# Optimization experiments

Measured on AMD Instinct MI355X. Metric: run time of the kernel, lower is better.

Reference implementation:

```python
import jax, jax.numpy as jnp
import numpy as np

P = 8.0  # Lp exponent of the distance neuron (finite-p stage of l_inf-dist training)


def _patches(t, k, stride, pad):
    # [B, Cin, H, W] -> [B, Cin*k*k, H', W'], feature dim ordered channel-major
    return jax.lax.conv_general_dilated_patches(
        t, (k, k), (stride, stride), [(pad, pad), (pad, pad)])


def _lp(d):
    # d: [B, Cout, Cin*k*k, H', W'] nonnegative -> Lp norm over patch dim
    return jnp.power(jnp.sum(jnp.power(d, P), axis=2), 1.0 / P)


def norm_dist_conv(x, l, u, w, stride, pad):
    # Lp-distance "convolution": y[b,o,i,j] = || patch(x)[b,:,i,j] - w[o,:] ||_p
    # mean_normalize=True: zero-center each output unit's weight vector
    Cout, Cin, k, _ = w.shape
    wf = w.reshape(Cout, -1)
    wf = wf - jnp.mean(wf, axis=1, keepdims=True)
    wb = wf[None, :, :, None, None]                      # [1, Cout, Ckk, 1, 1]
    px = _patches(x, k, stride, pad)[:, None]            # [B, 1, Ckk, H', W']
    pl = _patches(l, k, stride, pad)[:, None]
    pu = _patches(u, k, stride, pad)[:, None]
    y = _lp(jnp.abs(px - wb))
    # interval bounds of |x_j - w_j| given x_j in [l_j, u_j], then monotone Lp
    dl = jnp.maximum(jnp.maximum(pl - wb, wb - pu), 0.0)
    du = jnp.maximum(jnp.abs(pl - wb), jnp.abs(pu - wb))
    return y, _lp(dl), _lp(du)


def bound_relu(x, l, u):
    # ReLU is monotone: apply elementwise to value and both bounds
    return jax.nn.relu(x), jax.nn.relu(l), jax.nn.relu(u)


def setup_inputs() -> dict:
    key = jax.random.key(0)
    k1, k2, k3 = jax.random.split(key, 3)
    B, C, H, W = 4, 32, 32, 32
    eps = 0.1  # l_inf perturbation radius
    x = jax.random.normal(k1, (B, C, H, W), dtype=jnp.float32)
    lower = x - eps
    upper = x + eps
    scale = 1.0 / np.sqrt(C * 9)
    weight1 = jax.random.normal(k2, (C, C, 3, 3), dtype=jnp.float32) * scale
    weight2 = jax.random.normal(k3, (C, C, 3, 3), dtype=jnp.float32) * scale
    return {"x": x, "lower": lower, "upper": upper,
            "weight1": weight1, "weight2": weight2}


def reference(x, lower, upper, weight1, weight2):
    # conv1 (stride=1, pad=1) -> BoundReLU -> conv2 -> residual add -> BoundReLU
    o = norm_dist_conv(x, lower, upper, weight1, 1, 1)
    o = bound_relu(*o)
    o = norm_dist_conv(*o, weight2, 1, 1)
    out = (o[0] + x, o[1] + lower, o[2] + upper)  # identity shortcut (stride=1, in==out)
    out = bound_relu(*out)
    return jnp.stack(out)  # [3, B, C, H, W]: (value, lower, upper)
```

## Files before the change

### kernel.cpp

```cpp
#include <hip/hip_runtime.h>

#define NB 4
#define NC 32
#define NH 32
#define NW 32
#define KK 288
#define PLANE (NB*NC*NH*NW)
#define CHALF 16

__device__ __forceinline__ float s3(float v) { return sqrtf(sqrtf(sqrtf(v))); }

__global__ __launch_bounds__(256) void prep_weights_k(
        const float* __restrict__ w1, const float* __restrict__ w2,
        float* __restrict__ wf1, float* __restrict__ wf2)
{
    const int row = blockIdx.x;
    const float* src = (row < NC) ? w1 : w2;
    float* dst = (row < NC) ? wf1 : wf2;
    const int co = row & (NC - 1);
    const int tid = threadIdx.x;
    __shared__ float red[256];
    const float a = src[co*KK + tid];
    const float b = (tid + 256 < KK) ? src[co*KK + tid + 256] : 0.0f;
    red[tid] = a + b;
    __syncthreads();
    for (int s = 128; s > 0; s >>= 1) {
        if (tid < s) red[tid] += red[tid + s];
        __syncthreads();
    }
    const float mean = red[0] * (1.0f / (float)KK);
    {
        const int e = tid, c = e / 9, r9 = e - c*9, r = r9 / 3, kw = r9 - r*3;
        dst[co*384 + ((c*3 + r) << 2) + kw] = a - mean;
    }
    if (tid + 256 < KK) {
        const int e = tid + 256, c = e / 9, r9 = e - c*9, r = r9 / 3, kw = r9 - r*3;
        dst[co*384 + ((c*3 + r) << 2) + kw] = b - mean;
    }
}

template<bool STAGE2>
__global__ __launch_bounds__(256, 2) void normdist_conv_k(
    const float* __restrict__ sy,
    const float* __restrict__ sl,
    const float* __restrict__ su,
    const float* __restrict__ wf,
    float* __restrict__ pY, float* __restrict__ pL, float* __restrict__ pU)
{
    const int h     = blockIdx.x;
    const int cog   = blockIdx.y >> 1;
    const int chalf = blockIdx.y & 1;
    const int ch0   = chalf * CHALF;
    const int b     = blockIdx.z;
    const int tx    = threadIdx.x;
    const int ty    = threadIdx.y;
    const int tid   = ty * 32 + tx;

    __shared__ float4 sP[CHALF*3*34];

    for (int i = tid; i < CHALF*3*34; i += 256) {
        const int c   = i / 102;
        const int rem = i - c*102;
        const int r   = rem / 34;
        const int col = rem - r*34;
        const int gh  = h + r - 1;
        const int gw  = col - 1;
        float vx = 0.0f, vl = 0.0f, vu = 0.0f;
        if ((unsigned)gh < NH && (unsigned)gw < NW) {
            const int g = ((b*NC + ch0 + c)*NH + gh)*NW + gw;
            if (STAGE2) {
                vx = s3(sy[g] + sy[PLANE + g]);
                vl = s3(sl[g] + sl[PLANE + g]);
                vu = s3(su[g] + su[PLANE + g]);
            } else {
                vx = sy[g]; vl = sl[g]; vu = su[g];
            }
        }
        sP[i] = make_float4(vx, vl, vu, 0.0f);
    }
    __syncthreads();

    const int co0 = cog*16 + ty;
    const int co1 = co0 + 8;
    const float4* wbA = (const float4*)wf + (co0*NC + ch0)*3;
    const float4* wbB = (const float4*)wf + (co1*NC + ch0)*3;

    float aY0 = 0.0f, aL0 = 0.0f, aU0 = 0.0f;
    float aY1 = 0.0f, aL1 = 0.0f, aU1 = 0.0f;

    auto tap = [&](float wv, float4 p, float& accY, float& accL, float& accU) {
        const float d  = p.x - wv;
        const float d2 = d*d, d4 = d2*d2;
        accY = fmaf(d4, d4, accY);
        const float a  = p.y - wv;
        const float nb = wv - p.z;
        const float m  = fmaxf(fmaxf(a, nb), 0.0f);
        const float m2 = m*m, m4 = m2*m2;
        accL = fmaf(m4, m4, accL);
        const float a2 = a*a, q2 = nb*nb;
        const float mm2 = fmaxf(a2, q2);
        const float mm4 = mm2*mm2;
        accU = fmaf(mm4, mm4, accU);
    };

    float4 cA0 = wbA[0], cA1 = wbA[1], cA2 = wbA[2];
    float4 cB0 = wbB[0], cB1 = wbB[1], cB2 = wbB[2];

    for (int c = 0; c < CHALF; ++c) {
        const int cn = (c < CHALF-1) ? c + 1 : c;
        const float4 nA0 = wbA[cn*3+0], nA1 = wbA[cn*3+1], nA2 = wbA[cn*3+2];
        const float4 nB0 = wbB[cn*3+0], nB1 = wbB[cn*3+1], nB2 = wbB[cn*3+2];

        const int pb = c*102 + tx;
        const float4 p00 = sP[pb +  0], p01 = sP[pb +  1], p02 = sP[pb +  2];
        const float4 p10 = sP[pb + 34], p11 = sP[pb + 35], p12 = sP[pb + 36];
        const float4 p20 = sP[pb + 68], p21 = sP[pb + 69], p22 = sP[pb + 70];

        tap(cA0.x, p00, aY0, aL0, aU0); tap(cA0.y, p01, aY0, aL0, aU0); tap(cA0.z, p02, aY0, aL0, aU0);
        tap(cB0.x, p00, aY1, aL1, aU1); tap(cB0.y, p01, aY1, aL1, aU1); tap(cB0.z, p02, aY1, aL1, aU1);
        tap(cA1.x, p10, aY0, aL0, aU0); tap(cA1.y, p11, aY0, aL0, aU0); tap(cA1.z, p12, aY0, aL0, aU0);
        tap(cB1.x, p10, aY1, aL1, aU1); tap(cB1.y, p11, aY1, aL1, aU1); tap(cB1.z, p12, aY1, aL1, aU1);
        tap(cA2.x, p20, aY0, aL0, aU0); tap(cA2.y, p21, aY0, aL0, aU0); tap(cA2.z, p22, aY0, aL0, aU0);
        tap(cB2.x, p20, aY1, aL1, aU1); tap(cB2.y, p21, aY1, aL1, aU1); tap(cB2.z, p22, aY1, aL1, aU1);

        cA0 = nA0; cA1 = nA1; cA2 = nA2;
        cB0 = nB0; cB1 = nB1; cB2 = nB2;
    }

    const int o0 = ((b*NC + co0)*NH + h)*NW + tx;
    const int o1 = o0 + 8*NH*NW;
    pY[chalf*PLANE + o0] = aY0;
    pL[chalf*PLANE + o0] = aL0;
    pU[chalf*PLANE + o0] = aU0;
    pY[chalf*PLANE + o1] = aY1;
    pL[chalf*PLANE + o1] = aL1;
    pU[chalf*PLANE + o1] = aU1;
}

__global__ __launch_bounds__(256) void epilogue_k(
    const float* __restrict__ pY, const float* __restrict__ pL, const float* __restrict__ pU,
    const float* __restrict__ x,  const float* __restrict__ l,  const float* __restrict__ u,
    float* __restrict__ out)
{
    const int i = blockIdx.x*256 + threadIdx.x;
    const float4* pY4 = (const float4*)pY;
    const float4* pL4 = (const float4*)pL;
    const float4* pU4 = (const float4*)pU;
    const float4* x4  = (const float4*)x;
    const float4* l4  = (const float4*)l;
    const float4* u4  = (const float4*)u;
    float4* out4 = (float4*)out;
    const int Q = PLANE/4;

    const float4 ya = pY4[i], yb = pY4[Q + i];
    const float4 la = pL4[i], lb = pL4[Q + i];
    const float4 ua = pU4[i], ub = pU4[Q + i];
    const float4 xr = x4[i], lr = l4[i], ur = u4[i];

    float4 oy, ol, ou;
    oy.x = fmaxf(s3(ya.x + yb.x) + xr.x, 0.0f);
    oy.y = fmaxf(s3(ya.y + yb.y) + xr.y, 0.0f);
    oy.z = fmaxf(s3(ya.z + yb.z) + xr.z, 0.0f);
    oy.w = fmaxf(s3(ya.w + yb.w) + xr.w, 0.0f);
    ol.x = fmaxf(s3(la.x + lb.x) + lr.x, 0.0f);
    ol.y = fmaxf(s3(la.y + lb.y) + lr.y, 0.0f);
    ol.z = fmaxf(s3(la.z + lb.z) + lr.z, 0.0f);
    ol.w = fmaxf(s3(la.w + lb.w) + lr.w, 0.0f);
    ou.x = fmaxf(s3(ua.x + ub.x) + ur.x, 0.0f);
    ou.y = fmaxf(s3(ua.y + ub.y) + ur.y, 0.0f);
    ou.z = fmaxf(s3(ua.z + ub.z) + ur.z, 0.0f);
    ou.w = fmaxf(s3(ua.w + ub.w) + ur.w, 0.0f);

    out4[i]       = oy;
    out4[Q + i]   = ol;
    out4[2*Q + i] = ou;
}

extern "C" void kernel_launch(void* const* d_in, const int* in_sizes, int n_in,
                              void* d_out, int out_size, void* d_ws, size_t ws_size,
                              hipStream_t stream)
{
    const float* x  = (const float*)d_in[0];
    const float* l  = (const float*)d_in[1];
    const float* u  = (const float*)d_in[2];
    const float* w1 = (const float*)d_in[3];
    const float* w2 = (const float*)d_in[4];
    float* ws  = (float*)d_ws;
    float* wf1 = ws;
    float* wf2 = wf1 + 12288;
    float* p1Y = wf2 + 12288;
    float* p1L = p1Y + 2*PLANE;
    float* p1U = p1L + 2*PLANE;
    float* p2Y = p1U + 2*PLANE;
    float* p2L = p2Y + 2*PLANE;
    float* p2U = p2L + 2*PLANE;
    float* out = (float*)d_out;

    prep_weights_k<<<64, 256, 0, stream>>>(w1, w2, wf1, wf2);

    dim3 blk(32, 8);
    dim3 grd(NH, 4, NB);
    normdist_conv_k<false><<<grd, blk, 0, stream>>>(x, l, u, wf1, p1Y, p1L, p1U);
    normdist_conv_k<true ><<<grd, blk, 0, stream>>>(p1Y, p1L, p1U, wf2, p2Y, p2L, p2U);
    epilogue_k<<<PLANE/1024, 256, 0, stream>>>(p2Y, p2L, p2U, x, l, u, out);
}
```

Measured before the change: 108.0 us.

## Fuse all stages into one cooperative kernel with grid syncs

Combines weight prep, both distance-conv stages and the epilogue into a single cooperative launch of 256 blocks of 512 threads, separated by grid-wide syncs, to remove the cost of several kernel launches. Each block now covers all 32 output channels for one row and channel half, so the grid shrinks from 512 blocks of 256 threads to 256 blocks of 512. The epilogue becomes scalar rather than float4. If the cooperative launch fails, it falls back to separate kernels. With only 256 blocks the GPU may be underused, and grid syncs carry their own overhead.

```diff
diff --git a/kernel.cpp b/kernel.cpp
--- a/kernel.cpp
+++ b/kernel.cpp
@@ -1,4 +1,7 @@
 #include <hip/hip_runtime.h>
+#include <hip/hip_cooperative_groups.h>
+
+namespace cg = cooperative_groups;
 
 #define NB 4
 #define NC 32
@@ -7,58 +10,51 @@
 #define KK 288
 #define PLANE (NB*NC*NH*NW)
 #define CHALF 16
+#define NBLK 256
+#define NTHR 512
 
 __device__ __forceinline__ float s3(float v) { return sqrtf(sqrtf(sqrtf(v))); }
 
-__global__ __launch_bounds__(256) void prep_weights_k(
+
+__device__ __forceinline__ void prep_phase(int bid, int tid,
         const float* __restrict__ w1, const float* __restrict__ w2,
-        float* __restrict__ wf1, float* __restrict__ wf2)
-{
-    const int row = blockIdx.x;
-    const float* src = (row < NC) ? w1 : w2;
-    float* dst = (row < NC) ? wf1 : wf2;
-    const int co = row & (NC - 1);
-    const int tid = threadIdx.x;
-    __shared__ float red[256];
-    const float a = src[co*KK + tid];
-    const float b = (tid + 256 < KK) ? src[co*KK + tid + 256] : 0.0f;
-    red[tid] = a + b;
+        float* __restrict__ wf1, float* __restrict__ wf2, float* red)
+{
+    if (bid >= 2*NC) return;
+    const float* src = (bid < NC) ? w1 : w2;
+    float* dst = (bid < NC) ? wf1 : wf2;
+    const int co = bid & (NC - 1);
+    const float a = (tid < KK) ? src[co*KK + tid] : 0.0f;
+    red[tid] = a;
     __syncthreads();
-    for (int s = 128; s > 0; s >>= 1) {
+    for (int s = NTHR/2; s > 0; s >>= 1) {
         if (tid < s) red[tid] += red[tid + s];
         __syncthreads();
     }
     const float mean = red[0] * (1.0f / (float)KK);
-    {
-        const int e = tid, c = e / 9, r9 = e - c*9, r = r9 / 3, kw = r9 - r*3;
+    if (tid < KK) {
+        const int c = tid / 9, r9 = tid - c*9, r = r9 / 3, kw = r9 - r*3;
         dst[co*384 + ((c*3 + r) << 2) + kw] = a - mean;
     }
-    if (tid + 256 < KK) {
-        const int e = tid + 256, c = e / 9, r9 = e - c*9, r = r9 / 3, kw = r9 - r*3;
-        dst[co*384 + ((c*3 + r) << 2) + kw] = b - mean;
-    }
 }
 
 template<bool STAGE2>
-__global__ __launch_bounds__(256, 2) void normdist_conv_k(
+__device__ __forceinline__ void conv_phase(int bid, int tid,
     const float* __restrict__ sy,
     const float* __restrict__ sl,
     const float* __restrict__ su,
     const float* __restrict__ wf,
-    float* __restrict__ pY, float* __restrict__ pL, float* __restrict__ pU)
-{
-    const int h     = blockIdx.x;
-    const int cog   = blockIdx.y >> 1;
-    const int chalf = blockIdx.y & 1;
+    float* __restrict__ pY, float* __restrict__ pL, float* __restrict__ pU,
+    float4* sP)
+{
+    const int h     = bid & (NH - 1);
+    const int chalf = (bid >> 5) & 1;
+    const int b     = bid >> 6;
     const int ch0   = chalf * CHALF;
-    const int b     = blockIdx.z;
-    const int tx    = threadIdx.x;
-    const int ty    = threadIdx.y;
-    const int tid   = ty * 32 + tx;
-
-    __shared__ float4 sP[CHALF*3*34];
-
-    for (int i = tid; i < CHALF*3*34; i += 256) {
+    const int tx    = tid & 31;
+    const int ty    = tid >> 5;
+
+    for (int i = tid; i < CHALF*3*34; i += NTHR) {
         const int c   = i / 102;
         const int rem = i - c*102;
         const int r   = rem / 34;
@@ -80,8 +76,8 @@
     }
     __syncthreads();
 
-    const int co0 = cog*16 + ty;
-    const int co1 = co0 + 8;
+    const int co0 = ty;
+    const int co1 = ty + 16;
     const float4* wbA = (const float4*)wf + (co0*NC + ch0)*3;
     const float4* wbB = (const float4*)wf + (co1*NC + ch0)*3;
 
@@ -128,7 +124,7 @@
     }
 
     const int o0 = ((b*NC + co0)*NH + h)*NW + tx;
-    const int o1 = o0 + 8*NH*NW;
+    const int o1 = o0 + 16*NH*NW;
     pY[chalf*PLANE + o0] = aY0;
     pL[chalf*PLANE + o0] = aL0;
     pU[chalf*PLANE + o0] = aU0;
@@ -137,44 +133,76 @@
     pU[chalf*PLANE + o1] = aU1;
 }
 
-__global__ __launch_bounds__(256) void epilogue_k(
+__device__ __forceinline__ void epilogue_phase(int o,
     const float* __restrict__ pY, const float* __restrict__ pL, const float* __restrict__ pU,
     const float* __restrict__ x,  const float* __restrict__ l,  const float* __restrict__ u,
     float* __restrict__ out)
 {
-    const int i = blockIdx.x*256 + threadIdx.x;
-    const float4* pY4 = (const float4*)pY;
-    const float4* pL4 = (const float4*)pL;
-    const float4* pU4 = (const float4*)pU;
-    const float4* x4  = (const float4*)x;
-    const float4* l4  = (const float4*)l;
-    const float4* u4  = (const float4*)u;
-    float4* out4 = (float4*)out;
-    const int Q = PLANE/4;
-
-    const float4 ya = pY4[i], yb = pY4[Q + i];
-    const float4 la = pL4[i], lb = pL4[Q + i];
-    const float4 ua = pU4[i], ub = pU4[Q + i];
-    const float4 xr = x4[i], lr = l4[i], ur = u4[i];
-
-    float4 oy, ol, ou;
-    oy.x = fmaxf(s3(ya.x + yb.x) + xr.x, 0.0f);
-    oy.y = fmaxf(s3(ya.y + yb.y) + xr.y, 0.0f);
-    oy.z = fmaxf(s3(ya.z + yb.z) + xr.z, 0.0f);
-    oy.w = fmaxf(s3(ya.w + yb.w) + xr.w, 0.0f);
-    ol.x = fmaxf(s3(la.x + lb.x) + lr.x, 0.0f);
-    ol.y = fmaxf(s3(la.y + lb.y) + lr.y, 0.0f);
-    ol.z = fmaxf(s3(la.z + lb.z) + lr.z, 0.0f);
-    ol.w = fmaxf(s3(la.w + lb.w) + lr.w, 0.0f);
-    ou.x = fmaxf(s3(ua.x + ub.x) + ur.x, 0.0f);
-    ou.y = fmaxf(s3(ua.y + ub.y) + ur.y, 0.0f);
-    ou.z = fmaxf(s3(ua.z + ub.z) + ur.z, 0.0f);
-    ou.w = fmaxf(s3(ua.w + ub.w) + ur.w, 0.0f);
-
-    out4[i]       = oy;
-    out4[Q + i]   = ol;
-    out4[2*Q + i] = ou;
-}
+    const float y  = s3(pY[o] + pY[PLANE + o]);
+    const float dl = s3(pL[o] + pL[PLANE + o]);
+    const float du = s3(pU[o] + pU[PLANE + o]);
+    out[o]           = fmaxf(y  + x[o], 0.0f);
+    out[PLANE + o]   = fmaxf(dl + l[o], 0.0f);
+    out[2*PLANE + o] = fmaxf(du + u[o], 0.0f);
+}
+
+
+__global__ __launch_bounds__(NTHR, 1) void fused_k(
+    const float* __restrict__ x, const float* __restrict__ l, const float* __restrict__ u,
+    const float* __restrict__ w1, const float* __restrict__ w2,
+    float* __restrict__ wf1, float* __restrict__ wf2,
+    float* __restrict__ p1Y, float* __restrict__ p1L, float* __restrict__ p1U,
+    float* __restrict__ p2Y, float* __restrict__ p2L, float* __restrict__ p2U,
+    float* __restrict__ out)
+{
+    __shared__ float4 sP[CHALF*3*34];
+    __shared__ float red[NTHR];
+    cg::grid_group grid = cg::this_grid();
+    const int bid = blockIdx.x;
+    const int tid = threadIdx.x;
+
+    prep_phase(bid, tid, w1, w2, wf1, wf2, red);
+    __threadfence();
+    grid.sync();
+
+    conv_phase<false>(bid, tid, x, l, u, wf1, p1Y, p1L, p1U, sP);
+    __threadfence();
+    grid.sync();
+
+    conv_phase<true>(bid, tid, p1Y, p1L, p1U, wf2, p2Y, p2L, p2U, sP);
+    __threadfence();
+    grid.sync();
+
+    epilogue_phase(bid*NTHR + tid, p2Y, p2L, p2U, x, l, u, out);
+}
+
+
+__global__ __launch_bounds__(NTHR) void prep_only_k(
+        const float* __restrict__ w1, const float* __restrict__ w2,
+        float* __restrict__ wf1, float* __restrict__ wf2)
+{
+    __shared__ float red[NTHR];
+    prep_phase(blockIdx.x, threadIdx.x, w1, w2, wf1, wf2, red);
+}
+
+template<bool STAGE2>
+__global__ __launch_bounds__(NTHR) void conv_only_k(
+    const float* __restrict__ sy, const float* __restrict__ sl, const float* __restrict__ su,
+    const float* __restrict__ wf,
+    float* __restrict__ pY, float* __restrict__ pL, float* __restrict__ pU)
+{
+    __shared__ float4 sP[CHALF*3*34];
+    conv_phase<STAGE2>(blockIdx.x, threadIdx.x, sy, sl, su, wf, pY, pL, pU, sP);
+}
+
+__global__ __launch_bounds__(NTHR) void epilogue_only_k(
+    const float* __restrict__ pY, const float* __restrict__ pL, const float* __restrict__ pU,
+    const float* __restrict__ x,  const float* __restrict__ l,  const float* __restrict__ u,
+    float* __restrict__ out)
+{
+    epilogue_phase(blockIdx.x*NTHR + threadIdx.x, pY, pL, pU, x, l, u, out);
+}
+
 
 extern "C" void kernel_launch(void* const* d_in, const int* in_sizes, int n_in,
                               void* d_out, int out_size, void* d_ws, size_t ws_size,
@@ -196,11 +224,18 @@
     float* p2U = p2L + 2*PLANE;
     float* out = (float*)d_out;
 
-    prep_weights_k<<<64, 256, 0, stream>>>(w1, w2, wf1, wf2);
-
-    dim3 blk(32, 8);
-    dim3 grd(NH, 4, NB);
-    normdist_conv_k<false><<<grd, blk, 0, stream>>>(x, l, u, wf1, p1Y, p1L, p1U);
-    normdist_conv_k<true ><<<grd, blk, 0, stream>>>(p1Y, p1L, p1U, wf2, p2Y, p2L, p2U);
-    epilogue_k<<<PLANE/1024, 256, 0, stream>>>(p2Y, p2L, p2U, x, l, u, out);
-}
+    void* args[] = { (void*)&x, (void*)&l, (void*)&u, (void*)&w1, (void*)&w2,
+                     (void*)&wf1, (void*)&wf2,
+                     (void*)&p1Y, (void*)&p1L, (void*)&p1U,
+                     (void*)&p2Y, (void*)&p2L, (void*)&p2U, (void*)&out };
+
+    hipError_t err = hipLaunchCooperativeKernel((const void*)fused_k,
+                                                dim3(NBLK), dim3(NTHR), args, 0, stream);
+    if (err != hipSuccess) {
+        (void)hipGetLastError();
+        prep_only_k<<<2*NC, NTHR, 0, stream>>>(w1, w2, wf1, wf2);
+        conv_only_k<false><<<NBLK, NTHR, 0, stream>>>(x, l, u, wf1, p1Y, p1L, p1U);
+        conv_only_k<true ><<<NBLK, NTHR, 0, stream>>>(p1Y, p1L, p1U, wf2, p2Y, p2L, p2U);
+        epilogue_only_k<<<NBLK, NTHR, 0, stream>>>(p2Y, p2L, p2U, x, l, u, out);
+    }
+}
```

Result: slower. 335.0 us (+210.1%).

## Drop channel split-K and fuse Lp root plus residual epilogue into conv

Applied to the files above, without the earlier changes.

Each conv block now reduces over all 32 input channels instead of half. This removes the partial-sum buffers, the separate epilogue kernel, and the cross-half combine in stage 2's load. The 1/8 root, residual add and ReLU are applied directly when the second conv stores its result. In exchange the grid shrinks from 512 to 256 blocks, with twice the work per block and double the shared-memory tile. That lowers occupancy and may weaken latency hiding on a compute-bound loop.

```diff
diff --git a/kernel.cpp b/kernel.cpp
--- a/kernel.cpp
+++ b/kernel.cpp
@@ -6,7 +6,6 @@
 #define NW 32
 #define KK 288
 #define PLANE (NB*NC*NH*NW)
-#define CHALF 16
 
 __device__ __forceinline__ float s3(float v) { return sqrtf(sqrtf(sqrtf(v))); }
 
@@ -40,25 +39,22 @@
 }
 
 template<bool STAGE2>
-__global__ __launch_bounds__(256, 2) void normdist_conv_k(
-    const float* __restrict__ sy,
-    const float* __restrict__ sl,
-    const float* __restrict__ su,
+__global__ __launch_bounds__(256, 1) void conv_full_k(
+    const float* __restrict__ sy, const float* __restrict__ sl, const float* __restrict__ su,
     const float* __restrict__ wf,
-    float* __restrict__ pY, float* __restrict__ pL, float* __restrict__ pU)
+    const float* __restrict__ rx, const float* __restrict__ rl, const float* __restrict__ ru,
+    float* __restrict__ oY, float* __restrict__ oL, float* __restrict__ oU)
 {
-    const int h     = blockIdx.x;
-    const int cog   = blockIdx.y >> 1;
-    const int chalf = blockIdx.y & 1;
-    const int ch0   = chalf * CHALF;
-    const int b     = blockIdx.z;
-    const int tx    = threadIdx.x;
-    const int ty    = threadIdx.y;
-    const int tid   = ty * 32 + tx;
+    const int h   = blockIdx.x;
+    const int cog = blockIdx.y;
+    const int b   = blockIdx.z;
+    const int tx  = threadIdx.x;
+    const int ty  = threadIdx.y;
+    const int tid = ty * 32 + tx;
 
-    __shared__ float4 sP[CHALF*3*34];
+    __shared__ float4 sP[NC*3*34];
 
-    for (int i = tid; i < CHALF*3*34; i += 256) {
+    for (int i = tid; i < NC*3*34; i += 256) {
         const int c   = i / 102;
         const int rem = i - c*102;
         const int r   = rem / 34;
@@ -67,14 +63,8 @@
         const int gw  = col - 1;
         float vx = 0.0f, vl = 0.0f, vu = 0.0f;
         if ((unsigned)gh < NH && (unsigned)gw < NW) {
-            const int g = ((b*NC + ch0 + c)*NH + gh)*NW + gw;
-            if (STAGE2) {
-                vx = s3(sy[g] + sy[PLANE + g]);
-                vl = s3(sl[g] + sl[PLANE + g]);
-                vu = s3(su[g] + su[PLANE + g]);
-            } else {
-                vx = sy[g]; vl = sl[g]; vu = su[g];
-            }
+            const int g = ((b*NC + c)*NH + gh)*NW + gw;
+            vx = sy[g]; vl = sl[g]; vu = su[g];
         }
         sP[i] = make_float4(vx, vl, vu, 0.0f);
     }
@@ -82,8 +72,8 @@
 
     const int co0 = cog*16 + ty;
     const int co1 = co0 + 8;
-    const float4* wbA = (const float4*)wf + (co0*NC + ch0)*3;
-    const float4* wbB = (const float4*)wf + (co1*NC + ch0)*3;
+    const float4* wbA = (const float4*)wf + co0*NC*3;
+    const float4* wbB = (const float4*)wf + co1*NC*3;
 
     float aY0 = 0.0f, aL0 = 0.0f, aU0 = 0.0f;
     float aY1 = 0.0f, aL1 = 0.0f, aU1 = 0.0f;
@@ -106,8 +96,8 @@
     float4 cA0 = wbA[0], cA1 = wbA[1], cA2 = wbA[2];
     float4 cB0 = wbB[0], cB1 = wbB[1], cB2 = wbB[2];
 
-    for (int c = 0; c < CHALF; ++c) {
-        const int cn = (c < CHALF-1) ? c + 1 : c;
+    for (int c = 0; c < NC; ++c) {
+        const int cn = (c < NC-1) ? c + 1 : c;
         const float4 nA0 = wbA[cn*3+0], nA1 = wbA[cn*3+1], nA2 = wbA[cn*3+2];
         const float4 nB0 = wbB[cn*3+0], nB1 = wbB[cn*3+1], nB2 = wbB[cn*3+2];
 
@@ -129,51 +119,19 @@
 
     const int o0 = ((b*NC + co0)*NH + h)*NW + tx;
     const int o1 = o0 + 8*NH*NW;
-    pY[chalf*PLANE + o0] = aY0;
-    pL[chalf*PLANE + o0] = aL0;
-    pU[chalf*PLANE + o0] = aU0;
-    pY[chalf*PLANE + o1] = aY1;
-    pL[chalf*PLANE + o1] = aL1;
-    pU[chalf*PLANE + o1] = aU1;
-}
 
-__global__ __launch_bounds__(256) void epilogue_k(
-    const float* __restrict__ pY, const float* __restrict__ pL, const float* __restrict__ pU,
-    const float* __restrict__ x,  const float* __restrict__ l,  const float* __restrict__ u,
-    float* __restrict__ out)
-{
-    const int i = blockIdx.x*256 + threadIdx.x;
-    const float4* pY4 = (const float4*)pY;
-    const float4* pL4 = (const float4*)pL;
-    const float4* pU4 = (const float4*)pU;
-    const float4* x4  = (const float4*)x;
-    const float4* l4  = (const float4*)l;
-    const float4* u4  = (const float4*)u;
-    float4* out4 = (float4*)out;
-    const int Q = PLANE/4;
-
-    const float4 ya = pY4[i], yb = pY4[Q + i];
-    const float4 la = pL4[i], lb = pL4[Q + i];
-    const float4 ua = pU4[i], ub = pU4[Q + i];
-    const float4 xr = x4[i], lr = l4[i], ur = u4[i];
-
-    float4 oy, ol, ou;
-    oy.x = fmaxf(s3(ya.x + yb.x) + xr.x, 0.0f);
-    oy.y = fmaxf(s3(ya.y + yb.y) + xr.y, 0.0f);
-    oy.z = fmaxf(s3(ya.z + yb.z) + xr.z, 0.0f);
-    oy.w = fmaxf(s3(ya.w + yb.w) + xr.w, 0.0f);
-    ol.x = fmaxf(s3(la.x + lb.x) + lr.x, 0.0f);
-    ol.y = fmaxf(s3(la.y + lb.y) + lr.y, 0.0f);
-    ol.z = fmaxf(s3(la.z + lb.z) + lr.z, 0.0f);
-    ol.w = fmaxf(s3(la.w + lb.w) + lr.w, 0.0f);
-    ou.x = fmaxf(s3(ua.x + ub.x) + ur.x, 0.0f);
-    ou.y = fmaxf(s3(ua.y + ub.y) + ur.y, 0.0f);
-    ou.z = fmaxf(s3(ua.z + ub.z) + ur.z, 0.0f);
-    ou.w = fmaxf(s3(ua.w + ub.w) + ur.w, 0.0f);
-
-    out4[i]       = oy;
-    out4[Q + i]   = ol;
-    out4[2*Q + i] = ou;
+    if (STAGE2) {
+        oY[o0]         = fmaxf(s3(aY0) + rx[o0], 0.0f);
+        oY[o1]         = fmaxf(s3(aY1) + rx[o1], 0.0f);
+        oL[o0]         = fmaxf(s3(aL0) + rl[o0], 0.0f);
+        oL[o1]         = fmaxf(s3(aL1) + rl[o1], 0.0f);
+        oU[o0]         = fmaxf(s3(aU0) + ru[o0], 0.0f);
+        oU[o1]         = fmaxf(s3(aU1) + ru[o1], 0.0f);
+    } else {
+        oY[o0] = s3(aY0); oY[o1] = s3(aY1);
+        oL[o0] = s3(aL0); oL[o1] = s3(aL1);
+        oU[o0] = s3(aU0); oU[o1] = s3(aU1);
+    }
 }
 
 extern "C" void kernel_launch(void* const* d_in, const int* in_sizes, int n_in,
@@ -188,19 +146,19 @@
     float* ws  = (float*)d_ws;
     float* wf1 = ws;
     float* wf2 = wf1 + 12288;
-    float* p1Y = wf2 + 12288;
-    float* p1L = p1Y + 2*PLANE;
-    float* p1U = p1L + 2*PLANE;
-    float* p2Y = p1U + 2*PLANE;
-    float* p2L = p2Y + 2*PLANE;
-    float* p2U = p2L + 2*PLANE;
+    float* y1  = wf2 + 12288;
+    float* l1  = y1 + PLANE;
+    float* u1  = l1 + PLANE;
     float* out = (float*)d_out;
 
     prep_weights_k<<<64, 256, 0, stream>>>(w1, w2, wf1, wf2);
 
     dim3 blk(32, 8);
-    dim3 grd(NH, 4, NB);
-    normdist_conv_k<false><<<grd, blk, 0, stream>>>(x, l, u, wf1, p1Y, p1L, p1U);
-    normdist_conv_k<true ><<<grd, blk, 0, stream>>>(p1Y, p1L, p1U, wf2, p2Y, p2L, p2U);
-    epilogue_k<<<PLANE/1024, 256, 0, stream>>>(p2Y, p2L, p2U, x, l, u, out);
+    dim3 grd(NH, 2, NB);
+    conv_full_k<false><<<grd, blk, 0, stream>>>(x, l, u, wf1,
+                                                nullptr, nullptr, nullptr,
+                                                y1, l1, u1);
+    conv_full_k<true ><<<grd, blk, 0, stream>>>(y1, l1, u1, wf2,
+                                                x, l, u,
+                                                out, out + PLANE, out + 2*PLANE);
 }
```

New measurement: 112.1 us. 3.7% more time.

## Pack two output channels into v2f lanes for packed FP32 math

Applied to the files above, without the earlier changes.

The weight prep kernel now interleaves the weights of the paired output channels co and co+8 into adjacent slots. The inner distance loop can then run on two-wide float vectors with packed fma, mul and max, computing both channels' taps in one instruction stream. The aim is to roughly halve VALU instruction count in the compute-bound tap loop by using packed FP32 instructions. Risks are extra broadcast or move instructions, and packed max or sub lowering to scalar ops if the compiler does not emit v_pk forms for them.

```diff
diff --git a/kernel.cpp b/kernel.cpp
--- a/kernel.cpp
+++ b/kernel.cpp
@@ -8,7 +8,11 @@
 #define PLANE (NB*NC*NH*NW)
 #define CHALF 16
 
+typedef float v2f __attribute__((ext_vector_type(2)));
+
 __device__ __forceinline__ float s3(float v) { return sqrtf(sqrtf(sqrtf(v))); }
+__device__ __forceinline__ v2f pkfma(v2f a, v2f b, v2f c) { return __builtin_elementwise_fma(a, b, c); }
+__device__ __forceinline__ v2f pkmax(v2f a, v2f b) { return __builtin_elementwise_max(a, b); }
 
 __global__ __launch_bounds__(256) void prep_weights_k(
         const float* __restrict__ w1, const float* __restrict__ w2,
@@ -29,13 +33,15 @@
         __syncthreads();
     }
     const float mean = red[0] * (1.0f / (float)KK);
+    const int q    = ((co >> 4) << 3) | (co & 7);
+    const int slot = (co >> 3) & 1;
     {
         const int e = tid, c = e / 9, r9 = e - c*9, r = r9 / 3, kw = r9 - r*3;
-        dst[co*384 + ((c*3 + r) << 2) + kw] = a - mean;
+        dst[((q*NC + c)*3 + r)*8 + kw*2 + slot] = a - mean;
     }
     if (tid + 256 < KK) {
         const int e = tid + 256, c = e / 9, r9 = e - c*9, r = r9 / 3, kw = r9 - r*3;
-        dst[co*384 + ((c*3 + r) << 2) + kw] = b - mean;
+        dst[((q*NC + c)*3 + r)*8 + kw*2 + slot] = b - mean;
     }
 }
 
@@ -80,61 +86,58 @@
     }
     __syncthreads();
 
-    const int co0 = cog*16 + ty;
-    const int co1 = co0 + 8;
-    const float4* wbA = (const float4*)wf + (co0*NC + ch0)*3;
-    const float4* wbB = (const float4*)wf + (co1*NC + ch0)*3;
-
-    float aY0 = 0.0f, aL0 = 0.0f, aU0 = 0.0f;
-    float aY1 = 0.0f, aL1 = 0.0f, aU1 = 0.0f;
-
-    auto tap = [&](float wv, float4 p, float& accY, float& accL, float& accU) {
-        const float d  = p.x - wv;
-        const float d2 = d*d, d4 = d2*d2;
-        accY = fmaf(d4, d4, accY);
-        const float a  = p.y - wv;
-        const float nb = wv - p.z;
-        const float m  = fmaxf(fmaxf(a, nb), 0.0f);
-        const float m2 = m*m, m4 = m2*m2;
-        accL = fmaf(m4, m4, accL);
-        const float a2 = a*a, q2 = nb*nb;
-        const float mm2 = fmaxf(a2, q2);
-        const float mm4 = mm2*mm2;
-        accU = fmaf(mm4, mm4, accU);
+    const int q = cog*8 + ty;
+    const float4* wq = (const float4*)wf + (q*NC + ch0)*3*2;
+
+    v2f aY = {0.0f, 0.0f}, aL = {0.0f, 0.0f}, aU = {0.0f, 0.0f};
+
+    auto tap2 = [&](v2f w, const float4& p) {
+        const v2f px = {p.x, p.x};
+        const v2f py = {p.y, p.y};
+        const v2f pz = {p.z, p.z};
+        const v2f d  = px - w;
+        const v2f d2 = d*d, d4 = d2*d2;
+        aY = pkfma(d4, d4, aY);
+        const v2f a  = py - w;
+        const v2f nb = w - pz;
+        const v2f z  = {0.0f, 0.0f};
+        const v2f m  = pkmax(pkmax(a, nb), z);
+        const v2f m2 = m*m, m4 = m2*m2;
+        aL = pkfma(m4, m4, aL);
+        const v2f a2 = a*a, q2 = nb*nb;
+        const v2f mm2 = pkmax(a2, q2);
+        const v2f mm4 = mm2*mm2;
+        aU = pkfma(mm4, mm4, aU);
     };
 
-    float4 cA0 = wbA[0], cA1 = wbA[1], cA2 = wbA[2];
-    float4 cB0 = wbB[0], cB1 = wbB[1], cB2 = wbB[2];
+    float4 c0 = wq[0], c1 = wq[1], c2 = wq[2], c3 = wq[3], c4 = wq[4], c5 = wq[5];
 
     for (int c = 0; c < CHALF; ++c) {
         const int cn = (c < CHALF-1) ? c + 1 : c;
-        const float4 nA0 = wbA[cn*3+0], nA1 = wbA[cn*3+1], nA2 = wbA[cn*3+2];
-        const float4 nB0 = wbB[cn*3+0], nB1 = wbB[cn*3+1], nB2 = wbB[cn*3+2];
+        const float4 n0 = wq[cn*6+0], n1 = wq[cn*6+1], n2 = wq[cn*6+2];
+        const float4 n3 = wq[cn*6+3], n4 = wq[cn*6+4], n5 = wq[cn*6+5];
 
         const int pb = c*102 + tx;
         const float4 p00 = sP[pb +  0], p01 = sP[pb +  1], p02 = sP[pb +  2];
         const float4 p10 = sP[pb + 34], p11 = sP[pb + 35], p12 = sP[pb + 36];
         const float4 p20 = sP[pb + 68], p21 = sP[pb + 69], p22 = sP[pb + 70];
 
-        tap(cA0.x, p00, aY0, aL0, aU0); tap(cA0.y, p01, aY0, aL0, aU0); tap(cA0.z, p02, aY0, aL0, aU0);
-        tap(cB0.x, p00, aY1, aL1, aU1); tap(cB0.y, p01, aY1, aL1, aU1); tap(cB0.z, p02, aY1, aL1, aU1);
-        tap(cA1.x, p10, aY0, aL0, aU0); tap(cA1.y, p11, aY0, aL0, aU0); tap(cA1.z, p12, aY0, aL0, aU0);
-        tap(cB1.x, p10, aY1, aL1, aU1); tap(cB1.y, p11, aY1, aL1, aU1); tap(cB1.z, p12, aY1, aL1, aU1);
-        tap(cA2.x, p20, aY0, aL0, aU0); tap(cA2.y, p21, aY0, aL0, aU0); tap(cA2.z, p22, aY0, aL0, aU0);
-        tap(cB2.x, p20, aY1, aL1, aU1); tap(cB2.y, p21, aY1, aL1, aU1); tap(cB2.z, p22, aY1, aL1, aU1);
-
-        cA0 = nA0; cA1 = nA1; cA2 = nA2;
-        cB0 = nB0; cB1 = nB1; cB2 = nB2;
-    }
-
+        tap2((v2f){c0.x, c0.y}, p00); tap2((v2f){c0.z, c0.w}, p01); tap2((v2f){c1.x, c1.y}, p02);
+        tap2((v2f){c2.x, c2.y}, p10); tap2((v2f){c2.z, c2.w}, p11); tap2((v2f){c3.x, c3.y}, p12);
+        tap2((v2f){c4.x, c4.y}, p20); tap2((v2f){c4.z, c4.w}, p21); tap2((v2f){c5.x, c5.y}, p22);
+
+        c0 = n0; c1 = n1; c2 = n2; c3 = n3; c4 = n4; c5 = n5;
+    }
+
+    const int co0 = cog*16 + ty;
     const int o0 = ((b*NC + co0)*NH + h)*NW + tx;
     const int o1 = o0 + 8*NH*NW;
-    pY[chalf*PLANE + o0] = aY0;
-    pL[chalf*PLANE + o0] = aL0;
-    pU[chalf*PLANE + o0] = aU0;
-    pY[chalf*PLANE + o1] = aY1;
-    pL[chalf*PLANE + o1] = aL1;
-    pU[chalf*PLANE + o1] = aU1;
+    pY[chalf*PLANE + o0] = aY.x;
+    pL[chalf*PLANE + o0] = aL.x;
+    pU[chalf*PLANE + o0] = aU.x;
+    pY[chalf*PLANE + o1] = aY.y;
+    pL[chalf*PLANE + o1] = aL.y;
+    pU[chalf*PLANE + o1] = aU.y;
 }
 
 __global__ __launch_bounds__(256) void epilogue_k(
```

After: 103.0 us. 4.6% less time.
